# Kernel tuning notes

Measured on AMD Instinct MI355X. Metric: run time of the kernel, lower is better.

Reference implementation:

```python
import jax, jax.numpy as jnp
import numpy as np

B, T, C = 2, 2048, 1024
H, D = 16, 64
EPS = 1e-6


def _layernorm(x, gamma, beta):
    # Faithful to the torch module: uses unbiased std (Bessel) and divides by (std + eps).
    mean = x.mean(-1, keepdims=True)
    std = jnp.sqrt(jnp.sum((x - mean) ** 2, axis=-1, keepdims=True) / (x.shape[-1] - 1))
    return gamma * (x - mean) / (std + EPS) + beta


def setup_inputs() -> dict:
    key = jax.random.key(0)
    ks = jax.random.split(key, 9)
    s = lambda fan_in: 1.0 / np.sqrt(fan_in)
    return {
        "x": jax.random.normal(ks[0], (B, T, C), dtype=jnp.float32),
        "qkv_w": jax.random.uniform(ks[1], (3 * C, C), jnp.float32, -s(C), s(C)),
        "proj_w": jax.random.uniform(ks[2], (C, C), jnp.float32, -s(C), s(C)),
        "proj_b": jax.random.uniform(ks[3], (C,), jnp.float32, -s(C), s(C)),
        "l1_w": jax.random.uniform(ks[4], (4 * C, C), jnp.float32, -s(C), s(C)),
        "l1_b": jax.random.uniform(ks[5], (4 * C,), jnp.float32, -s(C), s(C)),
        "l3_w": jax.random.uniform(ks[6], (C, 4 * C), jnp.float32, -s(4 * C), s(4 * C)),
        "l3_b": jax.random.uniform(ks[7], (C,), jnp.float32, -s(4 * C), s(4 * C)),
        "ln1_g": jnp.ones((C,), jnp.float32),
        "ln1_b": jnp.zeros((C,), jnp.float32),
        "ln2_g": jnp.ones((C,), jnp.float32),
        "ln2_b": jnp.zeros((C,), jnp.float32),
    }


def _attention(x, qkv_w, proj_w, proj_b):
    Bx, Tx, Cx = x.shape
    qkv = x @ qkv_w.T                      # [B,T,3C]
    q, k, v = jnp.split(qkv, 3, axis=-1)
    q = q.reshape(Bx, Tx, H, D)
    k = k.reshape(Bx, Tx, H, D)
    v = v.reshape(Bx, Tx, H, D)
    scores = jnp.einsum("bthd,bshd->bhts", q, k) * (D ** -0.5)  # [B,H,T,T]
    causal = jnp.tril(jnp.ones((Tx, Tx), dtype=bool))
    scores = jnp.where(causal, scores, -jnp.inf)
    attn = jax.nn.softmax(scores, axis=-1)
    out = jnp.einsum("bhts,bshd->bthd", attn, v).reshape(Bx, Tx, Cx)
    return out @ proj_w.T + proj_b


def _mlp(x, l1_w, l1_b, l3_w, l3_b):
    h = jax.nn.relu(x @ l1_w.T + l1_b)     # [B,T,4C]
    return h @ l3_w.T + l3_b


def reference(x, qkv_w, proj_w, proj_b, l1_w, l1_b, l3_w, l3_b, ln1_g, ln1_b, ln2_g, ln2_b):
    # Dropout is identity in eval mode.
    x1 = x + _attention(_layernorm(x, ln1_g, ln1_b), qkv_w, proj_w, proj_b)
    x2 = x1 + _mlp(_layernorm(x1, ln2_g, ln2_b), l1_w, l1_b, l3_w, l3_b)
    return x2
```

## Files before the change

kernel.cpp:

```cpp
#include <hip/hip_runtime.h>

typedef unsigned short u16;
typedef short short8 __attribute__((ext_vector_type(8)));
typedef float floatx4 __attribute__((ext_vector_type(4)));

#define TT 2048
#define CC 1024
#define QSCALE 0.1803368801111244f
#define MFIX 32.0f

__device__ __forceinline__ u16 f2bf(float f) {
  return (u16)((__float_as_uint(f) + 0x8000u) >> 16);
}

__device__ __forceinline__ unsigned int pk2bf(float a, float b) {
  unsigned int ua = __float_as_uint(a) + 0x8000u;
  unsigned int ub = __float_as_uint(b) + 0x8000u;
  return __builtin_amdgcn_perm(ub, ua, 0x07060302u);
}

__device__ __forceinline__ void glds16(const u16* g, u16* l) {
  __builtin_amdgcn_global_load_lds((const __attribute__((address_space(1))) void*)g,
                                   (__attribute__((address_space(3))) void*)l, 16, 0, 0);
}

__device__ __forceinline__ void ln_body(const float* __restrict__ x,
                                        const float* __restrict__ g,
                                        const float* __restrict__ b,
                                        u16* __restrict__ out, int row, int tid) {
  const float4* xr = (const float4*)(x + (size_t)row * CC);
  float4 v = xr[tid];
  float s = v.x + v.y + v.z + v.w;
  float sq = v.x * v.x + v.y * v.y + v.z * v.z + v.w * v.w;
#pragma unroll
  for (int off = 1; off < 64; off <<= 1) {
    s += __shfl_xor(s, off);
    sq += __shfl_xor(sq, off);
  }
  __shared__ float ss[4], ssq[4];
  int wave = tid >> 6;
  if ((tid & 63) == 0) { ss[wave] = s; ssq[wave] = sq; }
  __syncthreads();
  s = ss[0] + ss[1] + ss[2] + ss[3];
  sq = ssq[0] + ssq[1] + ssq[2] + ssq[3];
  float mean = s * (1.0f / CC);
  float var = (sq - (float)CC * mean * mean) * (1.0f / (CC - 1));
  float inv = 1.0f / (sqrtf(fmaxf(var, 0.0f)) + 1e-6f);
  float4 gv = ((const float4*)g)[tid];
  float4 bv = ((const float4*)b)[tid];
  ushort4 o;
  o.x = f2bf(gv.x * (v.x - mean) * inv + bv.x);
  o.y = f2bf(gv.y * (v.y - mean) * inv + bv.y);
  o.z = f2bf(gv.z * (v.z - mean) * inv + bv.z);
  o.w = f2bf(gv.w * (v.w - mean) * inv + bv.w);
  ((ushort4*)(out + (size_t)row * CC))[tid] = o;
}

__global__ __launch_bounds__(256) void cvt_ln_kernel(const float* __restrict__ w0,
                                                     const float* __restrict__ w1,
                                                     const float* __restrict__ w2,
                                                     const float* __restrict__ w3,
                                                     const float* __restrict__ x,
                                                     const float* __restrict__ lg,
                                                     const float* __restrict__ lb,
                                                     u16* __restrict__ o0,
                                                     u16* __restrict__ o1,
                                                     u16* __restrict__ o2,
                                                     u16* __restrict__ o3,
                                                     u16* __restrict__ oln) {
  int blk = blockIdx.x;
  if (blk >= 12288) {
    ln_body(x, lg, lb, oln, blk - 12288, threadIdx.x);
    return;
  }
  const float* in;
  u16* out;
  int base;
  if (blk < 3072)      { in = w0; out = o0; base = 0; }
  else if (blk < 4096) { in = w1; out = o1; base = 3072; }
  else if (blk < 8192) { in = w2; out = o2; base = 4096; }
  else                 { in = w3; out = o3; base = 8192; }
  int i = (blk - base) * 256 + threadIdx.x;
  float4 v = ((const float4*)in)[i];
  ushort4 o;
  o.x = f2bf(v.x); o.y = f2bf(v.y); o.z = f2bf(v.z); o.w = f2bf(v.w);
  ((ushort4*)out)[i] = o;
}

__global__ __launch_bounds__(256) void ln_kernel(const float* __restrict__ x,
                                                 const float* __restrict__ g,
                                                 const float* __restrict__ b,
                                                 u16* __restrict__ out) {
  ln_body(x, g, b, out, blockIdx.x, threadIdx.x);
}


#define STAGE(tt)                                                         \
  {                                                                       \
    _Pragma("unroll") for (int g_ = 0; g_ < G; g_++)                      \
        glds16(gptr[g_] + (size_t)(tt) * 64, &lds[(tt) & 1][ldd[g_]]);    \
  }

#define BODY(t)                                                           \
  {                                                                       \
    asm volatile("s_waitcnt vmcnt(0)" ::: "memory");                      \
    __builtin_amdgcn_s_barrier();                                         \
    asm volatile("" ::: "memory");                                        \
    if ((t) + 1 < nst) STAGE((t) + 1);                                    \
    const u16* Ls = &lds[(t) & 1][0];                                     \
    _Pragma("unroll") for (int s_ = 0; s_ < 2; s_++) {                    \
      short8 bf[NJ];                                                      \
      _Pragma("unroll") for (int j_ = 0; j_ < NJ; j_++)                   \
          bf[j_] = *(const short8*)(Ls + (bOff[j_] ^ (s_ << 5)));         \
      _Pragma("unroll") for (int h_ = 0; h_ < MH; h_++) {                 \
        short8 af[MC];                                                    \
        _Pragma("unroll") for (int m_ = 0; m_ < MC; m_++)                 \
            af[m_] = *(const short8*)(Ls + (aOff[h_ * MC + m_] ^ (s_ << 5))); \
        if (s_ + h_ > 0) __builtin_amdgcn_s_barrier();                    \
        __builtin_amdgcn_s_setprio(1);                                    \
        _Pragma("unroll") for (int m_ = 0; m_ < MC; m_++)                 \
            _Pragma("unroll") for (int j_ = 0; j_ < NJ; j_++)             \
                acc[h_ * MC + m_][j_] = __builtin_amdgcn_mfma_f32_16x16x32_bf16( \
                    af[m_], bf[j_], acc[h_ * MC + m_][j_], 0, 0, 0);      \
        __builtin_amdgcn_s_setprio(0);                                    \
      }                                                                   \
    }                                                                     \
  }

template <int BM, int BN, int NWM, int NWN, int MODE>
__global__ __launch_bounds__(64 * NWM * NWN, 2) void gemmp(
    const u16* __restrict__ A, const u16* __restrict__ W,
    const float* __restrict__ bias, const float* __restrict__ resid,
    float* __restrict__ outf, u16* __restrict__ outb,
    int M, int N, int K) {
  constexpr int NW = NWM * NWN;
  constexpr int MI = BM / NWM / 16;
  constexpr int NJ = BN / NWN / 16;
  constexpr int ROWS = BM + BN;
  constexpr int G = ROWS / 8 / NW;
  constexpr int MH = (MI > 4) ? 2 : 1;
  constexpr int MC = MI / MH;
  static_assert(ROWS % (8 * NW) == 0, "chunk assignment");
  __shared__ u16 lds[2][ROWS * 64];

  const int tid = threadIdx.x;
  const int w = tid >> 6, lane = tid & 63;
  const int l15 = lane & 15, quad = lane >> 4;
  const int wm = (w / NWN) * (MI * 16);
  const int wn = (w % NWN) * (NJ * 16);
  const int tm = blockIdx.x * BM, tn = blockIdx.y * BN;

  const int srow = lane >> 3;
  const int xk = (lane & 7) ^ srow;
  const u16* gptr[G];
  int ldd[G];
#pragma unroll
  for (int g = 0; g < G; g++) {
    int c8 = (g * NW + w) * 8;
    const u16* rb = (c8 < BM) ? (A + (size_t)(tm + c8) * K)
                              : (W + (size_t)(tn + c8 - BM) * K);
    gptr[g] = rb + (size_t)srow * K + xk * 8;
    ldd[g] = c8 * 64;
  }

  int aOff[MI], bOff[NJ];
#pragma unroll
  for (int m = 0; m < MI; m++)
    aOff[m] = (wm + m * 16 + l15) * 64 + ((quad ^ (l15 & 7)) * 8);
#pragma unroll
  for (int j = 0; j < NJ; j++)
    bOff[j] = (BM + wn + j * 16 + l15) * 64 + ((quad ^ (l15 & 7)) * 8);

  floatx4 acc[MI][NJ];
#pragma unroll
  for (int m = 0; m < MI; m++)
#pragma unroll
    for (int j = 0; j < NJ; j++) acc[m][j] = (floatx4){0.f, 0.f, 0.f, 0.f};

  const int nst = K >> 6;

  STAGE(0);

#pragma unroll 2
  for (int t = 0; t < nst; ++t) BODY(t);

  float bb[NJ];
#pragma unroll
  for (int j = 0; j < NJ; j++)
    bb[j] = (MODE == 1 || MODE == 2) ? bias[tn + wn + j * 16 + l15] : 0.0f;
#pragma unroll
  for (int m = 0; m < MI; m++) {
    int row0 = tm + wm + m * 16 + quad * 4;
#pragma unroll
    for (int j = 0; j < NJ; j++) {
      int col = tn + wn + j * 16 + l15;
#pragma unroll
      for (int r = 0; r < 4; r++) {
        float v = acc[m][j][r];
        size_t idx = (size_t)(row0 + r) * N + col;
        if (MODE == 0) {
          if (col < 1024) v *= QSCALE;
          outb[idx] = f2bf(v);
        } else if (MODE == 1) {
          outf[idx] = v + bb[j] + resid[idx];
        } else {
          outb[idx] = f2bf(fmaxf(v + bb[j], 0.0f));
        }
      }
    }
  }
}

#undef STAGE
#undef BODY

__global__ __launch_bounds__(256) void flash_kernel(const u16* __restrict__ qkv,
                                                    u16* __restrict__ attn) {
  int bid = blockIdx.x;
  int qt = 31 - (bid >> 5);
  int bh = bid & 31;
  int b = bh >> 4, h = bh & 15;
  int tid = threadIdx.x, w = tid >> 6, lane = tid & 63;
  int l15 = lane & 15, quad = lane >> 4;

  __shared__ u16 k_lds[128 * 64];
  __shared__ u16 vt_lds[64 * 136];
  __shared__ u16 p_lds[4][16 * 136];

  int qbase = qt * 64 + w * 16;
  const u16* qp = qkv + (size_t)(b * TT + qbase + l15) * 3072 + h * 64;
  short8 qf0 = *(const short8*)(qp + quad * 8);
  short8 qf1 = *(const short8*)(qp + 32 + quad * 8);

  float l_i = 0.0f;
  floatx4 accO[4];
#pragma unroll
  for (int jf = 0; jf < 4; jf++) accO[jf] = (floatx4){0.f, 0.f, 0.f, 0.f};

  int rsub = lane >> 3;
  int cg = (lane & 7) ^ rsub;
  const u16* Kg = qkv + (size_t)(b * TT + w * 32 + rsub) * 3072 + 1024 + h * 64 + cg * 8;
  u16* kL = k_lds + w * 32 * 64;
  int s4 = (tid & 31) * 4;
  int dg = (tid >> 5) * 8;
  const u16* Vg = qkv + (size_t)(b * TT + s4) * 3072 + 2048 + h * 64 + dg;

  int x = l15 & 7;
  int kOff[8];
#pragma unroll
  for (int i = 0; i < 8; i++) kOff[i] = (i * 16 + l15) * 64 + ((quad ^ x) * 8);
  int pRd = l15 * 136 + quad * 8;

  int nt = (qt + 2) >> 1;
  for (int kt = 0; kt < nt; kt++) {
    int s0 = kt * 128;
    size_t soff = (size_t)s0 * 3072;
    uint4 R0 = *(const uint4*)(Vg + soff);
    uint4 R1 = *(const uint4*)(Vg + soff + 3072);
    uint4 R2 = *(const uint4*)(Vg + soff + 6144);
    uint4 R3 = *(const uint4*)(Vg + soff + 9216);
    __syncthreads();
#pragma unroll
    for (int is = 0; is < 4; is++) glds16(Kg + soff + (size_t)is * 8 * 3072, kL + is * 512);
    {
      unsigned int a0[4] = {R0.x, R0.y, R0.z, R0.w};
      unsigned int a1[4] = {R1.x, R1.y, R1.z, R1.w};
      unsigned int a2[4] = {R2.x, R2.y, R2.z, R2.w};
      unsigned int a3[4] = {R3.x, R3.y, R3.z, R3.w};
#pragma unroll
      for (int p = 0; p < 4; p++) {
        uint2 ev, od;
        ev.x = __builtin_amdgcn_perm(a1[p], a0[p], 0x05040100u);
        ev.y = __builtin_amdgcn_perm(a3[p], a2[p], 0x05040100u);
        od.x = __builtin_amdgcn_perm(a1[p], a0[p], 0x07060302u);
        od.y = __builtin_amdgcn_perm(a3[p], a2[p], 0x07060302u);
        *(uint2*)(vt_lds + (dg + 2 * p) * 136 + s4) = ev;
        *(uint2*)(vt_lds + (dg + 2 * p + 1) * 136 + s4) = od;
      }
    }
    __syncthreads();

    floatx4 st[8];
#pragma unroll
    for (int i = 0; i < 8; i++) st[i] = (floatx4){0.f, 0.f, 0.f, 0.f};
#pragma unroll
    for (int i = 0; i < 8; i++) {
      short8 kf0 = *(const short8*)(k_lds + kOff[i]);
      short8 kf1 = *(const short8*)(k_lds + (kOff[i] ^ 32));
      st[i] = __builtin_amdgcn_mfma_f32_16x16x32_bf16(kf0, qf0, st[i], 0, 0, 0);
      st[i] = __builtin_amdgcn_mfma_f32_16x16x32_bf16(kf1, qf1, st[i], 0, 0, 0);
    }

    if (s0 + 127 > qbase) {
      int mg = qbase + l15;
#pragma unroll
      for (int i = 0; i < 8; i++)
#pragma unroll
        for (int r = 0; r < 4; r++) {
          int s = s0 + i * 16 + quad * 4 + r;
          if (s > mg) st[i][r] = -3.0e38f;
        }
    }

    float ts = 0.0f;
#pragma unroll
    for (int i = 0; i < 8; i++)
#pragma unroll
      for (int r = 0; r < 4; r++) {
        float p = __builtin_amdgcn_exp2f(st[i][r] - MFIX);
        st[i][r] = p;
        ts += p;
      }
    ts += __shfl_xor(ts, 16);
    ts += __shfl_xor(ts, 32);
    l_i += ts;

#pragma unroll
    for (int i = 0; i < 8; i++) {
      uint2 pk;
      pk.x = pk2bf(st[i][0], st[i][1]);
      pk.y = pk2bf(st[i][2], st[i][3]);
      *(uint2*)(p_lds[w] + l15 * 136 + i * 16 + quad * 4) = pk;
    }

    short8 pf[4];
#pragma unroll
    for (int c = 0; c < 4; c++) pf[c] = *(const short8*)(p_lds[w] + pRd + c * 32);
#pragma unroll
    for (int jf = 0; jf < 4; jf++) {
      int vOff = (jf * 16 + l15) * 136 + quad * 8;
#pragma unroll
      for (int c = 0; c < 4; c++) {
        short8 vf = *(const short8*)(vt_lds + vOff + c * 32);
        accO[jf] = __builtin_amdgcn_mfma_f32_16x16x32_bf16(pf[c], vf, accO[jf], 0, 0, 0);
      }
    }
  }

  float invl = 1.0f / l_i;
  float iR[4];
#pragma unroll
  for (int r = 0; r < 4; r++) iR[r] = __shfl(invl, quad * 4 + r);
  int orow = b * TT + qbase + quad * 4;
#pragma unroll
  for (int r = 0; r < 4; r++) {
    u16* op = attn + (size_t)(orow + r) * CC + h * 64 + l15;
#pragma unroll
    for (int jf = 0; jf < 4; jf++) op[jf * 16] = f2bf(accO[jf][r] * iR[r]);
  }
}

extern "C" void kernel_launch(void* const* d_in, const int* in_sizes, int n_in,
                              void* d_out, int out_size, void* d_ws, size_t ws_size,
                              hipStream_t stream) {
  const float* x      = (const float*)d_in[0];
  const float* qkv_w  = (const float*)d_in[1];
  const float* proj_w = (const float*)d_in[2];
  const float* proj_b = (const float*)d_in[3];
  const float* l1_w   = (const float*)d_in[4];
  const float* l1_b   = (const float*)d_in[5];
  const float* l3_w   = (const float*)d_in[6];
  const float* l3_b   = (const float*)d_in[7];
  const float* ln1_g  = (const float*)d_in[8];
  const float* ln1_b  = (const float*)d_in[9];
  const float* ln2_g  = (const float*)d_in[10];
  const float* ln2_b  = (const float*)d_in[11];
  float* out = (float*)d_out;
  char* ws = (char*)d_ws;

  u16* w_qkv  = (u16*)(ws + 0);
  u16* w_proj = (u16*)(ws + 6291456);
  u16* w_l1   = (u16*)(ws + 8388608);
  u16* w_l3   = (u16*)(ws + 16777216);
  u16* lnb    = (u16*)(ws + 25165824);
  u16* qkvb   = (u16*)(ws + 33554432);
  u16* attnb  = (u16*)(ws + 58720256);
  float* x1   = (float*)(ws + 67108864);
  u16* hb     = (u16*)(ws + 83886080);

  cvt_ln_kernel<<<16384, 256, 0, stream>>>(qkv_w, proj_w, l1_w, l3_w, x, ln1_g, ln1_b,
                                           w_qkv, w_proj, w_l1, w_l3, lnb);
  gemmp<256, 256, 2, 4, 0><<<dim3(16, 12), 512, 0, stream>>>(
      lnb, w_qkv, nullptr, nullptr, nullptr, qkvb, 4096, 3072, 1024);
  flash_kernel<<<1024, 256, 0, stream>>>(qkvb, attnb);
  gemmp<128, 64, 2, 2, 1><<<dim3(32, 16), 256, 0, stream>>>(
      attnb, w_proj, proj_b, x, x1, nullptr, 4096, 1024, 1024);
  ln_kernel<<<4096, 256, 0, stream>>>(x1, ln2_g, ln2_b, lnb);
  gemmp<256, 256, 2, 4, 2><<<dim3(16, 16), 512, 0, stream>>>(
      lnb, w_l1, l1_b, nullptr, nullptr, hb, 4096, 4096, 1024);
  gemmp<128, 64, 2, 2, 1><<<dim3(32, 16), 256, 0, stream>>>(
      hb, w_l3, l3_b, x1, out, nullptr, 4096, 1024, 4096);
}
```

Measured before the change: 288.5 us.

## Use triple-buffered LDS ring with counted vmcnt for small GEMMs

Adds a DEPTH template parameter so the 128x64 GEMMs (proj and l3) prefetch two K-stages ahead into a three-slot LDS ring. They wait with a counted vmcnt(6) instead of draining all loads, so global loads overlap more of the compute. The intra-iteration barriers are also dropped for 4-wave blocks. The cost is more LDS per block, which could lower occupancy, and a hard-coded vmcnt literal that assumes G==6.

```diff
diff --git a/kernel.cpp b/kernel.cpp
--- a/kernel.cpp
+++ b/kernel.cpp
@@ -98,16 +98,16 @@
 #define STAGE(tt)                                                         \
   {                                                                       \
     _Pragma("unroll") for (int g_ = 0; g_ < G; g_++)                      \
-        glds16(gptr[g_] + (size_t)(tt) * 64, &lds[(tt) & 1][ldd[g_]]);    \
-  }
-
-#define BODY(t)                                                           \
+        glds16(gptr[g_] + (size_t)(tt) * 64, &lds[(tt) % RING][ldd[g_]]); \
+  }
+
+#define BODY(t, VM)                                                       \
   {                                                                       \
-    asm volatile("s_waitcnt vmcnt(0)" ::: "memory");                      \
+    asm volatile("s_waitcnt vmcnt(" #VM ")" ::: "memory");                \
     __builtin_amdgcn_s_barrier();                                         \
     asm volatile("" ::: "memory");                                        \
-    if ((t) + 1 < nst) STAGE((t) + 1);                                    \
-    const u16* Ls = &lds[(t) & 1][0];                                     \
+    if ((t) + DEPTH < nst) STAGE((t) + DEPTH);                            \
+    const u16* Ls = &lds[(t) % RING][0];                                  \
     _Pragma("unroll") for (int s_ = 0; s_ < 2; s_++) {                    \
       short8 bf[NJ];                                                      \
       _Pragma("unroll") for (int j_ = 0; j_ < NJ; j_++)                   \
@@ -116,7 +116,7 @@
         short8 af[MC];                                                    \
         _Pragma("unroll") for (int m_ = 0; m_ < MC; m_++)                 \
             af[m_] = *(const short8*)(Ls + (aOff[h_ * MC + m_] ^ (s_ << 5))); \
-        if (s_ + h_ > 0) __builtin_amdgcn_s_barrier();                    \
+        if (MIDB && (s_ + h_ > 0)) __builtin_amdgcn_s_barrier();          \
         __builtin_amdgcn_s_setprio(1);                                    \
         _Pragma("unroll") for (int m_ = 0; m_ < MC; m_++)                 \
             _Pragma("unroll") for (int j_ = 0; j_ < NJ; j_++)             \
@@ -127,7 +127,7 @@
     }                                                                     \
   }
 
-template <int BM, int BN, int NWM, int NWN, int MODE>
+template <int BM, int BN, int NWM, int NWN, int MODE, int DEPTH>
 __global__ __launch_bounds__(64 * NWM * NWN, 2) void gemmp(
     const u16* __restrict__ A, const u16* __restrict__ W,
     const float* __restrict__ bias, const float* __restrict__ resid,
@@ -140,8 +140,11 @@
   constexpr int G = ROWS / 8 / NW;
   constexpr int MH = (MI > 4) ? 2 : 1;
   constexpr int MC = MI / MH;
+  constexpr int RING = DEPTH + 1;
+  constexpr bool MIDB = (NW == 8);
   static_assert(ROWS % (8 * NW) == 0, "chunk assignment");
-  __shared__ u16 lds[2][ROWS * 64];
+  static_assert(DEPTH == 1 || G == 6, "counted vmcnt literal assumes G==6");
+  __shared__ u16 lds[RING][ROWS * 64];
 
   const int tid = threadIdx.x;
   const int w = tid >> 6, lane = tid & 63;
@@ -180,9 +183,16 @@
   const int nst = K >> 6;
 
   STAGE(0);
-
+  if constexpr (DEPTH == 2) STAGE(1);
+
+  if constexpr (DEPTH == 1) {
 #pragma unroll 2
-  for (int t = 0; t < nst; ++t) BODY(t);
+    for (int t = 0; t < nst; ++t) BODY(t, 0);
+  } else {
+#pragma unroll 3
+    for (int t = 0; t < nst - 1; ++t) BODY(t, 6);
+    BODY(nst - 1, 0);
+  }
 
   float bb[NJ];
 #pragma unroll
@@ -380,14 +390,14 @@
 
   cvt_ln_kernel<<<16384, 256, 0, stream>>>(qkv_w, proj_w, l1_w, l3_w, x, ln1_g, ln1_b,
                                            w_qkv, w_proj, w_l1, w_l3, lnb);
-  gemmp<256, 256, 2, 4, 0><<<dim3(16, 12), 512, 0, stream>>>(
+  gemmp<256, 256, 2, 4, 0, 1><<<dim3(16, 12), 512, 0, stream>>>(
       lnb, w_qkv, nullptr, nullptr, nullptr, qkvb, 4096, 3072, 1024);
   flash_kernel<<<1024, 256, 0, stream>>>(qkvb, attnb);
-  gemmp<128, 64, 2, 2, 1><<<dim3(32, 16), 256, 0, stream>>>(
+  gemmp<128, 64, 2, 2, 1, 2><<<dim3(32, 16), 256, 0, stream>>>(
       attnb, w_proj, proj_b, x, x1, nullptr, 4096, 1024, 1024);
   ln_kernel<<<4096, 256, 0, stream>>>(x1, ln2_g, ln2_b, lnb);
-  gemmp<256, 256, 2, 4, 2><<<dim3(16, 16), 512, 0, stream>>>(
+  gemmp<256, 256, 2, 4, 2, 1><<<dim3(16, 16), 512, 0, stream>>>(
       lnb, w_l1, l1_b, nullptr, nullptr, hb, 4096, 4096, 1024);
-  gemmp<128, 64, 2, 2, 1><<<dim3(32, 16), 256, 0, stream>>>(
+  gemmp<128, 64, 2, 2, 1, 2><<<dim3(32, 16), 256, 0, stream>>>(
       hb, w_l3, l3_b, x1, out, nullptr, 4096, 1024, 4096);
 }
```

New measurement: 298.5 us. 3.5% more time.
